# Kernel tuning notes

Hardware: AMD Instinct MI355X
Metric: run time of the kernel (lower is better)

Reference implementation:

```python
import jax, jax.numpy as jnp
import numpy as np

NUM_HEADS = 16
LN_EPS = 1e-05


def setup_inputs() -> dict:
    key = jax.random.key(0)
    ks = jax.random.split(key, 10)
    B, S, H = 2, 2048, 1024
    s = 1.0 / np.sqrt(H)
    return {
        "hidden_states": jax.random.normal(ks[0], (B, S, H), dtype=jnp.float32),
        "Wq": jax.random.normal(ks[1], (H, H), dtype=jnp.float32) * s,
        "bq": jax.random.normal(ks[2], (H,), dtype=jnp.float32) * 0.02,
        "Wk": jax.random.normal(ks[3], (H, H), dtype=jnp.float32) * s,
        "bk": jax.random.normal(ks[4], (H,), dtype=jnp.float32) * 0.02,
        "Wv": jax.random.normal(ks[5], (H, H), dtype=jnp.float32) * s,
        "bv": jax.random.normal(ks[6], (H,), dtype=jnp.float32) * 0.02,
        "Wd": jax.random.normal(ks[7], (H, H), dtype=jnp.float32) * s,
        "bd": jax.random.normal(ks[8], (H,), dtype=jnp.float32) * 0.02,
        "ln_gamma": jnp.ones((H,), dtype=jnp.float32),
        "ln_beta": jnp.zeros((H,), dtype=jnp.float32),
    }


def reference(hidden_states, Wq, bq, Wk, bk, Wv, bv, Wd, bd, ln_gamma, ln_beta):
    B, S, H = hidden_states.shape
    nh = NUM_HEADS
    hd = H // nh

    # QKV projections (torch Linear: x @ W.T + b), split heads -> [B, nh, S, hd]
    def proj(W, b):
        y = jnp.einsum('bsh,oh->bso', hidden_states, W) + b
        return y.reshape(B, S, nh, hd).transpose(0, 2, 1, 3)

    q = proj(Wq, bq)
    k = proj(Wk, bk)
    v = proj(Wv, bv)

    # scaled dot-product attention: [B, nh, S, S]
    scores = jnp.einsum('bhqd,bhkd->bhqk', q, k) / jnp.sqrt(jnp.float32(hd))
    probs = jax.nn.softmax(scores, axis=-1)
    ctx = jnp.einsum('bhqk,bhkd->bhqd', probs, v)  # [B, nh, S, hd]
    ctx = ctx.transpose(0, 2, 1, 3).reshape(B, S, H)

    # output dense + residual + LayerNorm
    attn_out = jnp.einsum('bsh,oh->bso', ctx, Wd) + bd
    x = attn_out + hidden_states
    mu = jnp.mean(x, axis=-1, keepdims=True)
    var = jnp.mean(jnp.square(x - mu), axis=-1, keepdims=True)
    return (x - mu) * jax.lax.rsqrt(var + LN_EPS) * ln_gamma + ln_beta
```

## Files before the change

### kernel.cpp

```cpp
#include <hip/hip_runtime.h>

constexpr int kH    = 1024;
constexpr int kSEQ  = 2048;
constexpr int kBATCH= 2;
constexpr int kNH   = 16;
constexpr int kHD   = 64;
constexpr int kM    = 4096;
constexpr int kSPLIT= 4;
constexpr int kKEYS = kSEQ / kSPLIT;

typedef _Float16 h8  __attribute__((ext_vector_type(8)));
typedef _Float16 h4  __attribute__((ext_vector_type(4)));
typedef float   f32x4  __attribute__((ext_vector_type(4)));
typedef float   f32x16 __attribute__((ext_vector_type(16)));

static __device__ __forceinline__ f32x4 mfma16(h8 a, h8 b, f32x4 c) {
  return __builtin_amdgcn_mfma_f32_16x16x32_f16(a, b, c, 0, 0, 0);
}
static __device__ __forceinline__ f32x16 mfma32(h8 a, h8 b, f32x16 c) {
  return __builtin_amdgcn_mfma_f32_32x32x16_f16(a, b, c, 0, 0, 0);
}

static __device__ __forceinline__ void gll16(const _Float16* g, _Float16* l) {
  __builtin_amdgcn_global_load_lds(
      (const __attribute__((address_space(1))) void*)g,
      (__attribute__((address_space(3))) void*)l, 16, 0, 0);
}

#define QSCALE 0.18033688011112042f
#define C0INIT (-5.770780163555854f)

__global__ __launch_bounds__(256) void cvt_all(
    const float* __restrict__ X,  const float* __restrict__ Wq,
    const float* __restrict__ Wk, const float* __restrict__ Wv,
    const float* __restrict__ Wd,
    _Float16* __restrict__ Xh,  _Float16* __restrict__ Wqh,
    _Float16* __restrict__ Wkh, _Float16* __restrict__ Wvh,
    _Float16* __restrict__ Wdh)
{
  int i = blockIdx.x * 256 + threadIdx.x;
  const float* src; _Float16* dst; int off;
  if (i < (kM * kH) / 4) {
    src = X; dst = Xh; off = i;
  } else {
    int j = i - (kM * kH) / 4;
    int w = j >> 18;
    off = j & 262143;
    src = (w == 0) ? Wq : (w == 1) ? Wk : (w == 2) ? Wv : Wd;
    dst = (w == 0) ? Wqh : (w == 1) ? Wkh : (w == 2) ? Wvh : Wdh;
  }
  float4 v = reinterpret_cast<const float4*>(src)[off];
  h4 o;
  o[0] = (_Float16)v.x; o[1] = (_Float16)v.y;
  o[2] = (_Float16)v.z; o[3] = (_Float16)v.w;
  reinterpret_cast<h4*>(dst)[off] = o;
}

__global__ __launch_bounds__(256, 2) void qkv_gemm(
    const _Float16* __restrict__ Xh,
    const _Float16* __restrict__ Wq, const _Float16* __restrict__ Wk,
    const _Float16* __restrict__ Wv,
    const float* __restrict__ bq, const float* __restrict__ bk,
    const float* __restrict__ bv,
    _Float16* __restrict__ Qo, _Float16* __restrict__ Ko, _Float16* __restrict__ Vo)
{
  const int proj = blockIdx.z;
  const _Float16* W   = (proj == 0) ? Wq : ((proj == 1) ? Wk : Wv);
  const float*    bias= (proj == 0) ? bq : ((proj == 1) ? bk : bv);
  _Float16*       Out = (proj == 0) ? Qo : ((proj == 1) ? Ko : Vo);

  const int m0 = blockIdx.y * 128, n0 = blockIdx.x * 128;
  __shared__ __align__(16) _Float16 As[2][128 * 32];
  __shared__ __align__(16) _Float16 Bs[2][128 * 32];

  const int tid  = threadIdx.x;
  const int wave = tid >> 6, lane = tid & 63, quad = lane >> 4, l16 = lane & 15;
  const int mw = (wave & 1) * 64, nw = (wave >> 1) * 64;

  f32x4 acc[4][4] = {};
  const int grow = wave * 32 + (lane >> 2);
  const int gcol = (lane & 3) * 8;
  const _Float16* Ag = Xh + (size_t)(m0 + grow) * kH + gcol;
  const _Float16* Bg = W  + (size_t)(n0 + grow) * kH + gcol;

  {
    gll16(Ag,            &As[0][wave * 1024]);
    gll16(Ag + 16 * kH,  &As[0][wave * 1024 + 512]);
    gll16(Bg,            &Bs[0][wave * 1024]);
    gll16(Bg + 16 * kH,  &Bs[0][wave * 1024 + 512]);
  }

  for (int k = 0; k < 32; ++k) {
    const int cur = k & 1;
    __syncthreads();
    if (k < 31) {
      const int k0 = (k + 1) * 32, nb = cur ^ 1;
      gll16(Ag + k0,           &As[nb][wave * 1024]);
      gll16(Ag + 16 * kH + k0, &As[nb][wave * 1024 + 512]);
      gll16(Bg + k0,           &Bs[nb][wave * 1024]);
      gll16(Bg + 16 * kH + k0, &Bs[nb][wave * 1024 + 512]);
    }
    h8 af[4], bf[4];
    #pragma unroll
    for (int mi = 0; mi < 4; ++mi)
      af[mi] = *reinterpret_cast<const h8*>(&As[cur][(mw + mi * 16 + l16) * 32 + quad * 8]);
    #pragma unroll
    for (int ni = 0; ni < 4; ++ni)
      bf[ni] = *reinterpret_cast<const h8*>(&Bs[cur][(nw + ni * 16 + l16) * 32 + quad * 8]);
    #pragma unroll
    for (int mi = 0; mi < 4; ++mi)
      #pragma unroll
      for (int ni = 0; ni < 4; ++ni)
        acc[mi][ni] = mfma16(af[mi], bf[ni], acc[mi][ni]);
  }

  #pragma unroll
  for (int mi = 0; mi < 4; ++mi)
  #pragma unroll
  for (int ni = 0; ni < 4; ++ni) {
    const int ng = n0 + nw + ni * 16 + l16;
    const float bv_ = bias[ng];
    const int hh = ng >> 6, dd = ng & 63;
    #pragma unroll
    for (int r = 0; r < 4; ++r) {
      const int mg = m0 + mw + mi * 16 + quad * 4 + r;
      float val = acc[mi][ni][r] + bv_;
      if (proj == 0) val *= QSCALE;
      const int bb = mg >> 11, srow = mg & 2047;
      Out[(((size_t)(bb * kNH + hh) * kSEQ) + srow) * kHD + dd] = (_Float16)val;
    }
  }
}

__global__ __launch_bounds__(256) void vtrans(const _Float16* __restrict__ V,
                                              _Float16* __restrict__ Vt)
{
  const int st = blockIdx.x;
  const int bh = blockIdx.y;
  __shared__ __align__(16) _Float16 Lt[64][72];
  const int t = threadIdx.x, r = t >> 2, c = (t & 3) * 16;
  const _Float16* src = V + (size_t)bh * kSEQ * kHD + (size_t)(st * 64 + r) * kHD + c;
  h8 p0 = *reinterpret_cast<const h8*>(src);
  h8 p1 = *reinterpret_cast<const h8*>(src + 8);
  #pragma unroll
  for (int e = 0; e < 8; ++e) Lt[c + e][r] = p0[e];
  #pragma unroll
  for (int e = 0; e < 8; ++e) Lt[c + 8 + e][r] = p1[e];
  __syncthreads();
  _Float16* dst = Vt + (size_t)bh * kHD * kSEQ + (size_t)r * kSEQ + st * 64 + c;
  *reinterpret_cast<h8*>(dst)     = *reinterpret_cast<const h8*>(&Lt[r][c]);
  *reinterpret_cast<h8*>(dst + 8) = *reinterpret_cast<const h8*>(&Lt[r][c + 8]);
}

__global__ __launch_bounds__(128, 2) void attn_kernel(
    const _Float16* __restrict__ Q, const _Float16* __restrict__ K,
    const _Float16* __restrict__ Vt, _Float16* __restrict__ Op,
    float* __restrict__ lp)
{
  const int qt = blockIdx.x, bh = blockIdx.y, split = blockIdx.z;
  const int tid = threadIdx.x;
  const int wave = tid >> 6, lane = tid & 63;
  const int quad = lane >> 4, l16 = lane & 15;
  const int lane32 = lane & 31, half = lane >> 5;

  __shared__ __align__(16) _Float16 Kl[2][64 * 64];
  __shared__ __align__(16) _Float16 Vl[2][64 * 64];
  __shared__ __align__(16) _Float16 Pl[2][32 * 64];

  const _Float16* Qb = Q  + (size_t)bh * kSEQ * kHD;
  const _Float16* Kb = K  + (size_t)bh * kSEQ * kHD;
  const _Float16* Vb = Vt + (size_t)bh * kHD * kSEQ;
  const int soff = split * kKEYS;
  const int qbase = qt * 128 + wave * 64;

  h8 qf[2][4];
  #pragma unroll
  for (int qc = 0; qc < 2; ++qc)
    #pragma unroll
    for (int kt = 0; kt < 4; ++kt)
      qf[qc][kt] = *reinterpret_cast<const h8*>(
          &Qb[(size_t)(qbase + qc * 32 + lane32) * kHD + kt * 16 + half * 8]);

  const int srow = lane >> 3;
  const int sch  = (lane & 7) ^ srow;
  const _Float16* Kg = Kb + (size_t)(soff + wave * 32 + srow) * kHD + sch * 8;
  const _Float16* Vg = Vb + (size_t)(wave * 32 + srow) * kSEQ + soff + sch * 8;

  f32x4 o[4][4] = {};
  float l_acc[2] = {0.f, 0.f};
  f32x16 cinit;
  #pragma unroll
  for (int r = 0; r < 16; ++r) cinit[r] = C0INIT;

  #pragma unroll
  for (int i = 0; i < 4; ++i) {
    gll16(Kg + i * 512,                 &Kl[0][(wave * 32 + i * 8) * 64]);
    gll16(Vg + (size_t)i * 8 * kSEQ,    &Vl[0][(wave * 32 + i * 8) * 64]);
  }

  for (int kt = 0; kt < kKEYS / 64; ++kt) {
    const int cur = kt & 1;
    __syncthreads();
    if (kt + 1 < kKEYS / 64) {
      const int nb = cur ^ 1;
      const int ko = (kt + 1) * 64;
      #pragma unroll
      for (int i = 0; i < 4; ++i) {
        gll16(Kg + (size_t)ko * kHD + i * 512,        &Kl[nb][(wave * 32 + i * 8) * 64]);
        gll16(Vg + (size_t)i * 8 * kSEQ + ko,         &Vl[nb][(wave * 32 + i * 8) * 64]);
      }
    }
    const _Float16* Kc = Kl[cur];
    const _Float16* Vc = Vl[cur];
    _Float16* PlW = Pl[wave];

    h8 ka[2][4];
    #pragma unroll
    for (int kc = 0; kc < 2; ++kc)
      #pragma unroll
      for (int dt = 0; dt < 4; ++dt)
        ka[kc][dt] = *reinterpret_cast<const h8*>(
            &Kc[(kc * 32 + lane32) * 64 + (((dt * 2 + half) ^ (lane32 & 7)) * 8)]);
    h8 vbf[4][2];
    #pragma unroll
    for (int dt = 0; dt < 4; ++dt)
      #pragma unroll
      for (int kc = 0; kc < 2; ++kc)
        vbf[dt][kc] = *reinterpret_cast<const h8*>(
            &Vc[(dt * 16 + l16) * 64 + (((kc * 4 + quad) ^ (l16 & 7)) * 8)]);

    #pragma unroll
    for (int qc = 0; qc < 2; ++qc) {
      f32x16 s0 = cinit, s1 = cinit;
      #pragma unroll
      for (int dt = 0; dt < 4; ++dt) s0 = mfma32(ka[0][dt], qf[qc][dt], s0);
      #pragma unroll
      for (int dt = 0; dt < 4; ++dt) s1 = mfma32(ka[1][dt], qf[qc][dt], s1);

      float la = 0.f;
      #pragma unroll
      for (int kc = 0; kc < 2; ++kc) {
        const f32x16& sv = kc ? s1 : s0;
        #pragma unroll
        for (int g = 0; g < 4; ++g) {
          float e0 = exp2f(sv[4 * g + 0]);
          float e1 = exp2f(sv[4 * g + 1]);
          float e2 = exp2f(sv[4 * g + 2]);
          float e3 = exp2f(sv[4 * g + 3]);
          la += (e0 + e1) + (e2 + e3);
          h4 pp;
          pp[0] = (_Float16)e0; pp[1] = (_Float16)e1;
          pp[2] = (_Float16)e2; pp[3] = (_Float16)e3;
          *reinterpret_cast<h4*>(
              &PlW[lane32 * 64 + (((kc * 4 + g) ^ (lane32 & 7)) * 8) + half * 4]) = pp;
        }
      }
      l_acc[qc] += la;

      h8 pa[2][2];
      #pragma unroll
      for (int qh = 0; qh < 2; ++qh)
        #pragma unroll
        for (int kc = 0; kc < 2; ++kc)
          pa[qh][kc] = *reinterpret_cast<const h8*>(
              &PlW[(qh * 16 + l16) * 64 + (((kc * 4 + quad) ^ (l16 & 7)) * 8)]);
      #pragma unroll
      for (int qh = 0; qh < 2; ++qh)
        #pragma unroll
        for (int dt = 0; dt < 4; ++dt) {
          o[qc * 2 + qh][dt] = mfma16(pa[qh][0], vbf[dt][0], o[qc * 2 + qh][dt]);
          o[qc * 2 + qh][dt] = mfma16(pa[qh][1], vbf[dt][1], o[qc * 2 + qh][dt]);
        }
    }
  }

  const size_t pbase = ((size_t)(split * (kBATCH * kNH) + bh)) * kSEQ;
  #pragma unroll
  for (int qc = 0; qc < 2; ++qc) {
    l_acc[qc] += __shfl_xor(l_acc[qc], 32);
    if (half == 0) lp[pbase + qbase + qc * 32 + lane32] = l_acc[qc];
  }
  #pragma unroll
  for (int qh = 0; qh < 4; ++qh)
    #pragma unroll
    for (int r = 0; r < 4; ++r) {
      const int q = qbase + qh * 16 + quad * 4 + r;
      #pragma unroll
      for (int dt = 0; dt < 4; ++dt)
        Op[(pbase + q) * kHD + dt * 16 + l16] = (_Float16)o[qh][dt][r];
    }
}

__global__ __launch_bounds__(256) void attn_merge(
    const _Float16* __restrict__ Op, const float* __restrict__ lp,
    _Float16* __restrict__ Ctx)
{
  const int t = blockIdx.x * 256 + threadIdx.x;
  const int d8 = t & 7, q = (t >> 3) & (kSEQ - 1), bh = t >> 14;
  float acc[8] = {};
  float l = 0.f;
  #pragma unroll
  for (int s = 0; s < kSPLIT; ++s) {
    const size_t pbase = ((size_t)(s * (kBATCH * kNH) + bh)) * kSEQ + q;
    h8 v = *reinterpret_cast<const h8*>(&Op[pbase * kHD + d8 * 8]);
    #pragma unroll
    for (int e = 0; e < 8; ++e) acc[e] += (float)v[e];
    l += lp[pbase];
  }
  const float inv = 1.f / l;
  const int b = bh >> 4, hh = bh & 15;
  h8 ov;
  #pragma unroll
  for (int e = 0; e < 8; ++e) ov[e] = (_Float16)(acc[e] * inv);
  *reinterpret_cast<h8*>(&Ctx[((size_t)(b * kSEQ + q)) * kH + hh * kHD + d8 * 8]) = ov;
}

__global__ __launch_bounds__(256, 2) void dense_gemm(
    const _Float16* __restrict__ A, const _Float16* __restrict__ W,
    const float* __restrict__ bias, const float* __restrict__ resid,
    float* __restrict__ Out)
{
  const int m0 = blockIdx.y * 128, n0 = blockIdx.x * 128;
  __shared__ __align__(16) _Float16 As[2][128 * 32];
  __shared__ __align__(16) _Float16 Bs[2][128 * 32];
  const int tid  = threadIdx.x;
  const int wave = tid >> 6, lane = tid & 63, quad = lane >> 4, l16 = lane & 15;
  const int mw = (wave & 1) * 64, nw = (wave >> 1) * 64;
  f32x4 acc[4][4] = {};
  const int grow = wave * 32 + (lane >> 2);
  const int gcol = (lane & 3) * 8;
  const _Float16* Ag = A + (size_t)(m0 + grow) * kH + gcol;
  const _Float16* Bg = W + (size_t)(n0 + grow) * kH + gcol;

  {
    gll16(Ag,           &As[0][wave * 1024]);
    gll16(Ag + 16 * kH, &As[0][wave * 1024 + 512]);
    gll16(Bg,           &Bs[0][wave * 1024]);
    gll16(Bg + 16 * kH, &Bs[0][wave * 1024 + 512]);
  }

  for (int k = 0; k < 32; ++k) {
    const int cur = k & 1;
    __syncthreads();
    if (k < 31) {
      const int k0 = (k + 1) * 32, nb = cur ^ 1;
      gll16(Ag + k0,           &As[nb][wave * 1024]);
      gll16(Ag + 16 * kH + k0, &As[nb][wave * 1024 + 512]);
      gll16(Bg + k0,           &Bs[nb][wave * 1024]);
      gll16(Bg + 16 * kH + k0, &Bs[nb][wave * 1024 + 512]);
    }
    h8 af[4], bf[4];
    #pragma unroll
    for (int mi = 0; mi < 4; ++mi)
      af[mi] = *reinterpret_cast<const h8*>(&As[cur][(mw + mi * 16 + l16) * 32 + quad * 8]);
    #pragma unroll
    for (int ni = 0; ni < 4; ++ni)
      bf[ni] = *reinterpret_cast<const h8*>(&Bs[cur][(nw + ni * 16 + l16) * 32 + quad * 8]);
    #pragma unroll
    for (int mi = 0; mi < 4; ++mi)
      #pragma unroll
      for (int ni = 0; ni < 4; ++ni)
        acc[mi][ni] = mfma16(af[mi], bf[ni], acc[mi][ni]);
  }
  #pragma unroll
  for (int mi = 0; mi < 4; ++mi)
  #pragma unroll
  for (int ni = 0; ni < 4; ++ni) {
    const int ng = n0 + nw + ni * 16 + l16;
    const float bv_ = bias[ng];
    #pragma unroll
    for (int r = 0; r < 4; ++r) {
      const int mg = m0 + mw + mi * 16 + quad * 4 + r;
      Out[(size_t)mg * kH + ng] = acc[mi][ni][r] + bv_ + resid[(size_t)mg * kH + ng];
    }
  }
}

__global__ __launch_bounds__(256) void ln_kernel(const float* __restrict__ Tmp,
    const float* __restrict__ gamma, const float* __restrict__ beta,
    float* __restrict__ out)
{
  const int row = blockIdx.x;
  const float4 v = reinterpret_cast<const float4*>(Tmp + (size_t)row * kH)[threadIdx.x];
  float s  = v.x + v.y + v.z + v.w;
  float ss = v.x * v.x + v.y * v.y + v.z * v.z + v.w * v.w;
  #pragma unroll
  for (int off = 32; off > 0; off >>= 1) {
    s  += __shfl_down(s, off);
    ss += __shfl_down(ss, off);
  }
  __shared__ float red[8];
  const int wave = threadIdx.x >> 6, lane = threadIdx.x & 63;
  if (lane == 0) { red[wave] = s; red[4 + wave] = ss; }
  __syncthreads();
  s  = red[0] + red[1] + red[2] + red[3];
  ss = red[4] + red[5] + red[6] + red[7];
  const float mu   = s * (1.f / kH);
  const float var  = ss * (1.f / kH) - mu * mu;
  const float rstd = rsqrtf(var + 1e-5f);
  const float4 g  = reinterpret_cast<const float4*>(gamma)[threadIdx.x];
  const float4 bb = reinterpret_cast<const float4*>(beta)[threadIdx.x];
  float4 o;
  o.x = (v.x - mu) * rstd * g.x + bb.x;
  o.y = (v.y - mu) * rstd * g.y + bb.y;
  o.z = (v.z - mu) * rstd * g.z + bb.z;
  o.w = (v.w - mu) * rstd * g.w + bb.w;
  reinterpret_cast<float4*>(out + (size_t)row * kH)[threadIdx.x] = o;
}

extern "C" void kernel_launch(void* const* d_in, const int* in_sizes, int n_in,
                              void* d_out, int out_size, void* d_ws, size_t ws_size,
                              hipStream_t stream) {
  const float* hs    = (const float*)d_in[0];
  const float* Wq    = (const float*)d_in[1];
  const float* bq    = (const float*)d_in[2];
  const float* Wk    = (const float*)d_in[3];
  const float* bk    = (const float*)d_in[4];
  const float* Wv    = (const float*)d_in[5];
  const float* bv    = (const float*)d_in[6];
  const float* Wd    = (const float*)d_in[7];
  const float* bd    = (const float*)d_in[8];
  const float* gamma = (const float*)d_in[9];
  const float* beta  = (const float*)d_in[10];
  float* out = (float*)d_out;

  char* ws = (char*)d_ws;
  _Float16* Xh   = (_Float16*)(ws + 0);
  _Float16* Wqh  = (_Float16*)(ws + 8388608);
  _Float16* Wkh  = (_Float16*)(ws + 10485760);
  _Float16* Wvh  = (_Float16*)(ws + 12582912);
  _Float16* Wdh  = (_Float16*)(ws + 14680064);
  _Float16* Qh   = (_Float16*)(ws + 16777216);
  _Float16* Kh   = (_Float16*)(ws + 25165824);
  _Float16* Vh   = (_Float16*)(ws + 33554432);
  _Float16* Vtb  = Xh;
  float*    lpart= (float*)Wqh;
  _Float16* Opart= (_Float16*)(ws + 33554432);
  _Float16* Ctx  = Qh;
  float*    Tmp  = (float*)(ws + 50331648);

  cvt_all<<<8192, 256, 0, stream>>>(hs, Wq, Wk, Wv, Wd, Xh, Wqh, Wkh, Wvh, Wdh);
  qkv_gemm<<<dim3(kH / 128, kM / 128, 3), 256, 0, stream>>>(
      Xh, Wqh, Wkh, Wvh, bq, bk, bv, Qh, Kh, Vh);
  vtrans<<<dim3(kSEQ / 64, kBATCH * kNH), 256, 0, stream>>>(Vh, Vtb);
  attn_kernel<<<dim3(kSEQ / 128, kBATCH * kNH, kSPLIT), 128, 0, stream>>>(
      Qh, Kh, Vtb, Opart, lpart);
  attn_merge<<<2048, 256, 0, stream>>>(Opart, lpart, Ctx);
  dense_gemm<<<dim3(kH / 128, kM / 128), 256, 0, stream>>>(Ctx, Wdh, bd, hs, Tmp);
  ln_kernel<<<kM, 256, 0, stream>>>(Tmp, gamma, beta, out);
}
```

Measured before the change: 234.7 us.

## Stage QKV epilogue through LDS and widen attention blocks to four waves

The QKV GEMM epilogue now writes results into swizzled shared memory and then emits coalesced 16-byte row stores into the head-split layout, replacing scattered 2-byte stores. The attention kernel grows from 2 to 4 waves per block (256 query rows), so each K/V tile loaded into LDS is shared by twice as many query rows and the load work per wave is halved. The costs are extra LDS traffic and barriers in the epilogue, a larger per-block LDS footprint, and half as many attention blocks, which may lower occupancy or load balance.

Result: no change. 238.7 us (+1.7%).

```diff
diff --git a/kernel.cpp b/kernel.cpp
--- a/kernel.cpp
+++ b/kernel.cpp
@@ -114,20 +114,40 @@
         acc[mi][ni] = mfma16(af[mi], bf[ni], acc[mi][ni]);
   }
 
+  __syncthreads();
+  _Float16* Crows = (mw == 0) ? &As[0][0] : &Bs[0][0];
   #pragma unroll
   for (int mi = 0; mi < 4; ++mi)
   #pragma unroll
   for (int ni = 0; ni < 4; ++ni) {
-    const int ng = n0 + nw + ni * 16 + l16;
-    const float bv_ = bias[ng];
-    const int hh = ng >> 6, dd = ng & 63;
+    const int col = nw + ni * 16 + l16;
+    const float bv_ = bias[n0 + col];
     #pragma unroll
     for (int r = 0; r < 4; ++r) {
-      const int mg = m0 + mw + mi * 16 + quad * 4 + r;
+      const int rr = mi * 16 + quad * 4 + r;
       float val = acc[mi][ni][r] + bv_;
       if (proj == 0) val *= QSCALE;
-      const int bb = mg >> 11, srow = mg & 2047;
-      Out[(((size_t)(bb * kNH + hh) * kSEQ) + srow) * kHD + dd] = (_Float16)val;
+      const int chunk = (col >> 3) ^ (rr & 7);
+      Crows[rr * 128 + chunk * 8 + (col & 7)] = (_Float16)val;
+    }
+  }
+  __syncthreads();
+  {
+    const int r = tid >> 1;
+    const int halfc = tid & 1;
+    const _Float16* base = (r < 64) ? &As[0][0] : &Bs[0][0];
+    const int rr = r & 63;
+    const int mg = m0 + r;
+    const int bb = mg >> 11, srow = mg & 2047;
+    const int ng0 = n0 + halfc * 64;
+    const int hh = ng0 >> 6;
+    _Float16* dst = Out + (((size_t)(bb * kNH + hh) * kSEQ) + srow) * kHD;
+    #pragma unroll
+    for (int c8 = 0; c8 < 8; ++c8) {
+      const int col0 = halfc * 64 + c8 * 8;
+      const int chunk = (col0 >> 3) ^ (rr & 7);
+      h8 v = *reinterpret_cast<const h8*>(&base[rr * 128 + chunk * 8]);
+      *reinterpret_cast<h8*>(dst + c8 * 8) = v;
     }
   }
 }
@@ -152,7 +172,7 @@
   *reinterpret_cast<h8*>(dst + 8) = *reinterpret_cast<const h8*>(&Lt[r][c + 8]);
 }
 
-__global__ __launch_bounds__(128, 2) void attn_kernel(
+__global__ __launch_bounds__(256, 2) void attn_kernel(
     const _Float16* __restrict__ Q, const _Float16* __restrict__ K,
     const _Float16* __restrict__ Vt, _Float16* __restrict__ Op,
     float* __restrict__ lp)
@@ -165,13 +185,13 @@
 
   __shared__ __align__(16) _Float16 Kl[2][64 * 64];
   __shared__ __align__(16) _Float16 Vl[2][64 * 64];
-  __shared__ __align__(16) _Float16 Pl[2][32 * 64];
+  __shared__ __align__(16) _Float16 Pl[4][32 * 64];
 
   const _Float16* Qb = Q  + (size_t)bh * kSEQ * kHD;
   const _Float16* Kb = K  + (size_t)bh * kSEQ * kHD;
   const _Float16* Vb = Vt + (size_t)bh * kHD * kSEQ;
   const int soff = split * kKEYS;
-  const int qbase = qt * 128 + wave * 64;
+  const int qbase = qt * 256 + wave * 64;
 
   h8 qf[2][4];
   #pragma unroll
@@ -183,8 +203,8 @@
 
   const int srow = lane >> 3;
   const int sch  = (lane & 7) ^ srow;
-  const _Float16* Kg = Kb + (size_t)(soff + wave * 32 + srow) * kHD + sch * 8;
-  const _Float16* Vg = Vb + (size_t)(wave * 32 + srow) * kSEQ + soff + sch * 8;
+  const _Float16* Kg = Kb + (size_t)(soff + wave * 16 + srow) * kHD + sch * 8;
+  const _Float16* Vg = Vb + (size_t)(wave * 16 + srow) * kSEQ + soff + sch * 8;
 
   f32x4 o[4][4] = {};
   float l_acc[2] = {0.f, 0.f};
@@ -193,9 +213,9 @@
   for (int r = 0; r < 16; ++r) cinit[r] = C0INIT;
 
   #pragma unroll
-  for (int i = 0; i < 4; ++i) {
-    gll16(Kg + i * 512,                 &Kl[0][(wave * 32 + i * 8) * 64]);
-    gll16(Vg + (size_t)i * 8 * kSEQ,    &Vl[0][(wave * 32 + i * 8) * 64]);
+  for (int i = 0; i < 2; ++i) {
+    gll16(Kg + (size_t)i * 8 * kHD,     &Kl[0][(wave * 16 + i * 8) * 64]);
+    gll16(Vg + (size_t)i * 8 * kSEQ,    &Vl[0][(wave * 16 + i * 8) * 64]);
   }
 
   for (int kt = 0; kt < kKEYS / 64; ++kt) {
@@ -205,9 +225,9 @@
       const int nb = cur ^ 1;
       const int ko = (kt + 1) * 64;
       #pragma unroll
-      for (int i = 0; i < 4; ++i) {
-        gll16(Kg + (size_t)ko * kHD + i * 512,        &Kl[nb][(wave * 32 + i * 8) * 64]);
-        gll16(Vg + (size_t)i * 8 * kSEQ + ko,         &Vl[nb][(wave * 32 + i * 8) * 64]);
+      for (int i = 0; i < 2; ++i) {
+        gll16(Kg + (size_t)(ko + i * 8) * kHD,      &Kl[nb][(wave * 16 + i * 8) * 64]);
+        gll16(Vg + (size_t)i * 8 * kSEQ + ko,       &Vl[nb][(wave * 16 + i * 8) * 64]);
       }
     }
     const _Float16* Kc = Kl[cur];
@@ -443,7 +463,7 @@
   qkv_gemm<<<dim3(kH / 128, kM / 128, 3), 256, 0, stream>>>(
       Xh, Wqh, Wkh, Wvh, bq, bk, bv, Qh, Kh, Vh);
   vtrans<<<dim3(kSEQ / 64, kBATCH * kNH), 256, 0, stream>>>(Vh, Vtb);
-  attn_kernel<<<dim3(kSEQ / 128, kBATCH * kNH, kSPLIT), 128, 0, stream>>>(
+  attn_kernel<<<dim3(kSEQ / 256, kBATCH * kNH, kSPLIT), 256, 0, stream>>>(
       Qh, Kh, Vtb, Opart, lpart);
   attn_merge<<<2048, 256, 0, stream>>>(Opart, lpart, Ctx);
   dense_gemm<<<dim3(kH / 128, kM / 128), 256, 0, stream>>>(Ctx, Wdh, bd, hs, Tmp);
```
